# Optimization experiments

Measured on AMD Instinct MI355X. Metric: run time of the kernel, lower is better.

Reference implementation:

```python
import jax, jax.numpy as jnp
import numpy as np

HIDDEN = 2048
NUM_HEADS = 32
HEAD_DIM = 64
NUM_KV = 8
GROUP = NUM_HEADS // NUM_KV
SCALE = HEAD_DIM ** -0.5
ROPE_BASE = 10000.0


def apply_rope(t):
    # t: [B, H, S, D]; standard half-split rotary embedding
    S, D = t.shape[-2], t.shape[-1]
    inv_freq = 1.0 / (ROPE_BASE ** (jnp.arange(0, D, 2, dtype=jnp.float32) / D))  # [D/2]
    ang = jnp.arange(S, dtype=jnp.float32)[:, None] * inv_freq[None, :]           # [S, D/2]
    cos, sin = jnp.cos(ang), jnp.sin(ang)
    x1, x2 = t[..., : D // 2], t[..., D // 2 :]
    return jnp.concatenate([x1 * cos - x2 * sin, x2 * cos + x1 * sin], axis=-1)


def setup_inputs() -> dict:
    key = jax.random.key(0)
    ks = jax.random.split(key, 10)
    B, S = 2, 2048
    s_in = HIDDEN ** -0.5
    s_o = (NUM_HEADS * HEAD_DIM) ** -0.5
    return {
        "x": jax.random.normal(ks[0], (B, S, HIDDEN), jnp.float32),
        "Wq": jax.random.normal(ks[1], (NUM_HEADS * HEAD_DIM, HIDDEN), jnp.float32) * s_in,
        "bq": jnp.zeros((NUM_HEADS * HEAD_DIM,), jnp.float32),
        "Wk": jax.random.normal(ks[2], (NUM_KV * HEAD_DIM, HIDDEN), jnp.float32) * s_in,
        "bk": jnp.zeros((NUM_KV * HEAD_DIM,), jnp.float32),
        "Wv": jax.random.normal(ks[3], (NUM_KV * HEAD_DIM, HIDDEN), jnp.float32) * s_in,
        "bv": jnp.zeros((NUM_KV * HEAD_DIM,), jnp.float32),
        "Wo": jax.random.normal(ks[4], (HIDDEN, NUM_HEADS * HEAD_DIM), jnp.float32) * s_o,
        "bo": jnp.zeros((HIDDEN,), jnp.float32),
        "key_weights": jax.random.normal(ks[5], (NUM_HEADS,), jnp.float32),
    }


def reference(x, Wq, bq, Wk, bk, Wv, bv, Wo, bo, key_weights):
    B, S, _ = x.shape
    q = (x @ Wq.T + bq).reshape(B, S, NUM_HEADS, HEAD_DIM).transpose(0, 2, 1, 3)
    k = (x @ Wk.T + bk).reshape(B, S, NUM_KV, HEAD_DIM).transpose(0, 2, 1, 3)
    v = (x @ Wv.T + bv).reshape(B, S, NUM_KV, HEAD_DIM).transpose(0, 2, 1, 3)
    q = apply_rope(q)
    k = apply_rope(k)
    # group queries per KV head: [B, kv, g, S, D]
    qg = q.reshape(B, NUM_KV, GROUP, S, HEAD_DIM)
    scores = jnp.einsum("bkgsd,bktd->bkgst", qg, k) * SCALE
    scores = scores * key_weights.reshape(1, NUM_KV, GROUP, 1, 1)
    causal = jnp.tril(jnp.ones((S, S), bool))
    scores = jnp.where(causal, scores, -jnp.inf)
    a = jax.nn.softmax(scores, axis=-1)
    o = jnp.einsum("bkgst,bktd->bkgsd", a, v)  # [B, kv, g, S, D]
    o = o.reshape(B, NUM_HEADS, S, HEAD_DIM).transpose(0, 2, 1, 3).reshape(B, S, NUM_HEADS * HEAD_DIM)
    return o @ Wo.T + bo
```

## Files before the change

### kernel.cpp

```cpp
#include <hip/hip_runtime.h>
#include <stdint.h>

#define S_LEN 2048
#define HID   2048
#define NH    32
#define NKV   8
#define HD    64
#define BATCH 2
#define NROWS (BATCH * S_LEN)
#define QKVN  (NH*HD + 2*NKV*HD)

typedef unsigned short u16;
typedef __bf16 bf16_t;
typedef bf16_t bf16x8 __attribute__((ext_vector_type(8)));
typedef float  f32x4  __attribute__((ext_vector_type(4)));
typedef float  f32x16 __attribute__((ext_vector_type(16)));
typedef u16    u16x8  __attribute__((ext_vector_type(8)));

#define LOG2E 1.4426950408889634f

__device__ __forceinline__ u16 f2bf(float f) {
    union { float f; uint32_t u; } v; v.f = f;
    uint32_t u = v.u;
    return (u16)((u + 0x7fffu + ((u >> 16) & 1u)) >> 16);
}

__device__ __forceinline__ unsigned cvtpk(float a, float b) {
    unsigned r;
    asm("v_cvt_pk_bf16_f32 %0, %1, %2" : "=v"(r) : "v"(a), "v"(b));
    return r;
}

__device__ __forceinline__ void plswap(unsigned &a, unsigned &b) {
    asm volatile("v_permlane32_swap_b32 %0, %1" : "+v"(a), "+v"(b));
}

__device__ __forceinline__ void llds16(const void* g, void* l) {
    __builtin_amdgcn_global_load_lds(
        (const __attribute__((address_space(1))) void*)g,
        (__attribute__((address_space(3))) void*)l,
        16, 0, 0);
}

#define CBAR(N) do { \
    asm volatile("s_waitcnt vmcnt(" #N ")" ::: "memory"); \
    __builtin_amdgcn_s_barrier(); \
    __builtin_amdgcn_sched_barrier(0); \
} while (0)

#define CVT_GROUPS 2359296
__global__ void prep_all(const float* __restrict__ x, const float* __restrict__ wq,
                         const float* __restrict__ wk, const float* __restrict__ wv,
                         const float* __restrict__ wo,
                         const float* __restrict__ bq, const float* __restrict__ bk,
                         const float* __restrict__ bv,
                         u16* __restrict__ xb, u16* __restrict__ wqkvb, u16* __restrict__ wob,
                         float* __restrict__ rtab, float* __restrict__ bqkv) {
    int e = blockIdx.x * 256 + threadIdx.x;
    if (e < CVT_GROUPS) {
        const float* s; u16* d; int o;
        if (e < 1048576)      { s = x;  d = xb;                 o = e; }
        else if (e < 1572864) { s = wq; d = wqkvb;              o = e - 1048576; }
        else if (e < 1703936) { s = wk; d = wqkvb + 2048*2048;  o = e - 1572864; }
        else if (e < 1835008) { s = wv; d = wqkvb + 2560*2048;  o = e - 1703936; }
        else                  { s = wo; d = wob;                o = e - 1835008; }
        const float4* sp = (const float4*)s;
        float4 a = sp[2*(size_t)o], b = sp[2*(size_t)o + 1];
        u16x8 r;
        r[0]=f2bf(a.x); r[1]=f2bf(a.y); r[2]=f2bf(a.z); r[3]=f2bf(a.w);
        r[4]=f2bf(b.x); r[5]=f2bf(b.y); r[6]=f2bf(b.z); r[7]=f2bf(b.w);
        *(u16x8*)(d + 8*(size_t)o) = r;
    } else if (e < CVT_GROUPS + 65536) {
        int idx = e - CVT_GROUPS;
        int i = idx & 31, s = idx >> 5;
        float invf = exp2f(-(float)i * (13.287712379549449f / 32.0f));
        float ang = (float)s * invf;
        float sn, cs;
        sincosf(ang, &sn, &cs);
        rtab[idx] = cs;
        rtab[S_LEN*32 + idx] = sn;
    } else if (e < CVT_GROUPS + 65536 + QKVN) {
        int i = e - CVT_GROUPS - 65536;
        bqkv[i] = (i < 2048) ? bq[i] : (i < 2560 ? bk[i - 2048] : bv[i - 2560]);
    }
}


__global__ __launch_bounds__(256, 2) void gemm_qkv(
    const u16* __restrict__ A, const u16* __restrict__ Bw,
    const float* __restrict__ bias, const float* __restrict__ rtab,
    const float* __restrict__ kw,
    u16* __restrict__ qpk, u16* __restrict__ kpk, u16* __restrict__ vlin)
{
    const int M = NROWS, N = QKVN, K = HID;
    const int nbm = M >> 7, nbn = N >> 8;
    const int nwg = nbm * nbn;
    int wg = blockIdx.x;
    wg = (wg & 7) * (nwg >> 3) + (wg >> 3);
    const int bm = wg % nbm, bn = wg / nbm;
    const int brow = bm << 7, bcol = bn << 8;

    __shared__ u16 sbuf[3][12288];

    const int t = threadIdx.x;
    const int lane = t & 63, wid = t >> 6;
    const int wr = wid >> 1, wn = wid & 1;
    const int lr = lane & 15, lhi = lane >> 4;

    auto stage = [&](int kt, int bi) {
        const int k0 = kt << 5;
        #pragma unroll
        for (int i = 0; i < 2; ++i) {
            const unsigned off = ((unsigned)t << 4) + ((unsigned)i << 12);
            const unsigned row = off >> 6;
            const unsigned scb = (off & 63) ^ ((row & 3) << 4);
            llds16(A + (size_t)(brow + row) * K + (k0 + (scb >> 1)), &sbuf[bi][0] + (off >> 1));
        }
        #pragma unroll
        for (int i = 0; i < 4; ++i) {
            const unsigned off = ((unsigned)t << 4) + ((unsigned)i << 12);
            const unsigned row = off >> 6;
            const unsigned scb = (off & 63) ^ ((row & 3) << 4);
            llds16(Bw + (size_t)(bcol + row) * K + (k0 + (scb >> 1)), &sbuf[bi][4096] + (off >> 1));
        }
    };

    f32x4 acc[4][8] = {};
    const int nk = K >> 5;

    stage(0, 0);
    stage(1, 1);
    int cur = 0, st2 = 2;
    for (int kt = 0; kt < nk; ++kt) {
        if (kt < nk - 1) CBAR(6); else CBAR(0);
        if (kt + 2 < nk) stage(kt + 2, st2);
        const char* sA = (const char*)&sbuf[cur][0];
        const char* sB = (const char*)&sbuf[cur][4096];
        bf16x8 af[4], bfv[8];
        #pragma unroll
        for (int m = 0; m < 4; ++m) {
            const int row = wr*64 + m*16 + lr;
            af[m] = *(const bf16x8*)(sA + row*64 + ((lhi*16) ^ ((row & 3) << 4)));
        }
        #pragma unroll
        for (int n = 0; n < 8; ++n) {
            const int row = wn*128 + n*16 + lr;
            bfv[n] = *(const bf16x8*)(sB + row*64 + ((lhi*16) ^ ((row & 3) << 4)));
        }
        #pragma unroll
        for (int m = 0; m < 4; ++m)
            #pragma unroll
            for (int n = 0; n < 8; ++n)
                acc[m][n] = __builtin_amdgcn_mfma_f32_16x16x32_bf16(af[m], bfv[n], acc[m][n], 0, 0, 0);
        cur = (cur == 2) ? 0 : cur + 1;
        st2 = (st2 == 2) ? 0 : st2 + 1;
    }

    const int rowb = brow + wr*64;
    #pragma unroll
    for (int hg = 0; hg < 2; ++hg) {
        const int c64 = bcol + wn*128 + hg*64;
        const int hb  = c64 >> 6;
        if (hb < 40) {
            const bool isQ = hb < 32;
            const float sc = isQ ? (0.125f * LOG2E * kw[hb]) : 1.0f;
            u16* dst = isQ ? qpk : kpk;
            const int nheads = isQ ? 32 : 8;
            const int hloc = isQ ? hb : (hb - 32);
            #pragma unroll
            for (int m = 0; m < 4; ++m) {
                #pragma unroll
                for (int nn = 0; nn < 2; ++nn) {
                    const int n = 4*hg + nn;
                    const int i = nn*16 + lr;
                    const float b1 = bias[c64 + i];
                    const float b2 = bias[c64 + i + 32];
                    #pragma unroll
                    for (int j = 0; j < 4; ++j) {
                        const int row = rowb + m*16 + lhi*4 + j;
                        const int s = row & (S_LEN - 1);
                        const int bb = row >> 11;
                        const float x1 = acc[m][n][j] + b1;
                        const float x2 = acc[m][n+2][j] + b2;
                        const float cs = rtab[s*32 + i];
                        const float sn = rtab[S_LEN*32 + s*32 + i];
                        const size_t base = ((size_t)(bb*nheads + hloc)) * (S_LEN*64) + (size_t)s*64;
                        dst[base + i]      = f2bf((x1*cs - x2*sn) * sc);
                        dst[base + i + 32] = f2bf((x2*cs + x1*sn) * sc);
                    }
                }
            }
        } else {
            #pragma unroll
            for (int m = 0; m < 4; ++m) {
                #pragma unroll
                for (int nn = 0; nn < 4; ++nn) {
                    const int col = c64 + nn*16 + lr;
                    const float bv = bias[col];
                    #pragma unroll
                    for (int j = 0; j < 4; ++j) {
                        const int row = rowb + m*16 + lhi*4 + j;
                        vlin[(size_t)row * 512 + (col - 2560)] = f2bf(acc[m][nn + 4*hg][j] + bv);
                    }
                }
            }
        }
    }
}

__global__ __launch_bounds__(256, 2) void gemm_bt(
    const u16* __restrict__ A, const u16* __restrict__ Bw,
    const float* __restrict__ bias, float* __restrict__ C,
    int M, int N, int K)
{
    const int nbm = M >> 7, nbn = N >> 8;
    const int nwg = nbm * nbn;
    int wg = blockIdx.x;
    wg = (wg & 7) * (nwg >> 3) + (wg >> 3);
    const int bm = wg % nbm, bn = wg / nbm;
    const int brow = bm << 7, bcol = bn << 8;

    __shared__ u16 sbuf[3][12288];

    const int t = threadIdx.x;
    const int lane = t & 63, wid = t >> 6;
    const int wr = wid >> 1, wn = wid & 1;
    const int lr = lane & 15, lhi = lane >> 4;

    auto stage = [&](int kt, int bi) {
        const int k0 = kt << 5;
        #pragma unroll
        for (int i = 0; i < 2; ++i) {
            const unsigned off = ((unsigned)t << 4) + ((unsigned)i << 12);
            const unsigned row = off >> 6;
            const unsigned scb = (off & 63) ^ ((row & 3) << 4);
            llds16(A + (size_t)(brow + row) * K + (k0 + (scb >> 1)), &sbuf[bi][0] + (off >> 1));
        }
        #pragma unroll
        for (int i = 0; i < 4; ++i) {
            const unsigned off = ((unsigned)t << 4) + ((unsigned)i << 12);
            const unsigned row = off >> 6;
            const unsigned scb = (off & 63) ^ ((row & 3) << 4);
            llds16(Bw + (size_t)(bcol + row) * K + (k0 + (scb >> 1)), &sbuf[bi][4096] + (off >> 1));
        }
    };

    f32x4 acc[4][8] = {};
    const int nk = K >> 5;

    stage(0, 0);
    stage(1, 1);
    int cur = 0, st2 = 2;
    for (int kt = 0; kt < nk; ++kt) {
        if (kt < nk - 1) CBAR(6); else CBAR(0);
        if (kt + 2 < nk) stage(kt + 2, st2);
        const char* sA = (const char*)&sbuf[cur][0];
        const char* sB = (const char*)&sbuf[cur][4096];
        bf16x8 af[4], bfv[8];
        #pragma unroll
        for (int m = 0; m < 4; ++m) {
            const int row = wr*64 + m*16 + lr;
            af[m] = *(const bf16x8*)(sA + row*64 + ((lhi*16) ^ ((row & 3) << 4)));
        }
        #pragma unroll
        for (int n = 0; n < 8; ++n) {
            const int row = wn*128 + n*16 + lr;
            bfv[n] = *(const bf16x8*)(sB + row*64 + ((lhi*16) ^ ((row & 3) << 4)));
        }
        #pragma unroll
        for (int m = 0; m < 4; ++m)
            #pragma unroll
            for (int n = 0; n < 8; ++n)
                acc[m][n] = __builtin_amdgcn_mfma_f32_16x16x32_bf16(af[m], bfv[n], acc[m][n], 0, 0, 0);
        cur = (cur == 2) ? 0 : cur + 1;
        st2 = (st2 == 2) ? 0 : st2 + 1;
    }

    #pragma unroll
    for (int m = 0; m < 4; ++m) {
        #pragma unroll
        for (int n = 0; n < 8; ++n) {
            const int col = bcol + wn*128 + n*16 + lr;
            const float bv = bias[col];
            #pragma unroll
            for (int j = 0; j < 4; ++j) {
                const int row = brow + wr*64 + m*16 + lhi*4 + j;
                C[(size_t)row * N + col] = acc[m][n][j] + bv;
            }
        }
    }
}

__global__ void pack_vt(const u16* __restrict__ vlin, u16* __restrict__ vtb) {
    __shared__ u16 tile[64][67];
    const int st = blockIdx.x;
    const int bk = blockIdx.y;
    const int t = threadIdx.x;
    const int b = bk >> 3, kvh = bk & 7;
    const int r = t >> 2, cg = (t & 3) << 4;
    const u16* src = vlin + ((size_t)(b*S_LEN + st*64 + r)) * 512 + kvh*64 + cg;
    #pragma unroll
    for (int j = 0; j < 16; ++j) tile[r][cg + j] = src[j];
    __syncthreads();
    const int d = t >> 2, sg = (t & 3) << 4;
    u16* dst = vtb + ((size_t)(bk*64 + d)) * S_LEN + st*64 + sg;
    #pragma unroll
    for (int j = 0; j < 16; ++j) dst[j] = tile[sg + j][d];
}

__global__ __launch_bounds__(512, 4) void attn_fwd(
    const u16* __restrict__ Q,
    const u16* __restrict__ Kk,
    const u16* __restrict__ Vt,
    u16* __restrict__ O)
{
    __shared__ u16 sK[3][64 * 64];
    __shared__ u16 sV[3][64 * 64];

    const int t = threadIdx.x;
    const int lane = t & 63, wid = t >> 6;
    const int hi = lane >> 5, lq = lane & 31;
    const int bid = blockIdx.x;
    const int qb = (bid < 256) ? (7 - (bid >> 6)) : ((bid >> 6) - 4);
    const int bh = bid & 63;
    const int b = bh >> 5, h = bh & 31;
    const int kvh = h >> 2;

    const u16* Kp = Kk + ((size_t)(b*NKV + kvh)) * (S_LEN * 64);
    const u16* Vp = Vt + ((size_t)(b*NKV + kvh)) * (64 * S_LEN);

    const int q0w = qb*256 + wid*32;
    const int qg  = q0w + lq;

    const u16* Qrow = Q + (((size_t)bh) * S_LEN + qg) * 64 + 8*hi;
    bf16x8 qf[4];
    #pragma unroll
    for (int kd = 0; kd < 4; ++kd)
        qf[kd] = *(const bf16x8*)(Qrow + 16*kd);

    f32x16 accO0 = {}, accO1 = {};
    float m_run = 0.f, l_run = 0.f;

    const int ntB = 4*qb + 4;
    const int tmax_w = (q0w + 31) >> 6;

    auto stageKV = [&](int kt, int bi) {
        const int kv = kt << 6;
        const unsigned row = t >> 3, cb = (t & 7) << 4;
        const unsigned scb = cb ^ ((row & 7) << 4);
        llds16(Kp + (size_t)(kv + row) * 64 + (scb >> 1), &sK[bi][0] + t*8);
        llds16(Vp + (size_t)row * S_LEN + kv + (scb >> 1), &sV[bi][0] + t*8);
    };

    stageKV(0, 0);
    stageKV(1, 1);
    int cur = 0, st2 = 2;

    for (int tt = 0; tt < ntB; ++tt) {
        if (tt < ntB - 1) CBAR(2); else CBAR(0);
        if (tt + 2 < ntB) stageKV(tt + 2, st2);
        if (tt <= tmax_w) {
            const int kv0 = tt * 64;
            const float nm = -m_run;
            f32x16 s0, s1;
            #pragma unroll
            for (int r = 0; r < 16; ++r) { s0[r] = nm; s1[r] = nm; }
            #pragma unroll
            for (int kd = 0; kd < 4; ++kd) {
                const unsigned bc = ((unsigned)(32*kd + 16*hi)) ^ ((lq & 7) << 4);
                bf16x8 k0 = *(const bf16x8*)((const char*)&sK[cur][0] + lq*128 + bc);
                bf16x8 k1 = *(const bf16x8*)((const char*)&sK[cur][0] + (32 + lq)*128 + bc);
                s0 = __builtin_amdgcn_mfma_f32_32x32x16_bf16(k0, qf[kd], s0, 0, 0, 0);
                s1 = __builtin_amdgcn_mfma_f32_32x32x16_bf16(k1, qf[kd], s1, 0, 0, 0);
            }
            if (kv0 + 63 > q0w) {
                #pragma unroll
                for (int r = 0; r < 16; ++r) {
                    const int kvg = kv0 + (r & 3) + 8*(r >> 2) + 4*hi;
                    if (kvg > qg)      s0[r] = -INFINITY;
                    if (kvg + 32 > qg) s1[r] = -INFINITY;
                }
            }
            float mx[8];
            #pragma unroll
            for (int r = 0; r < 8; ++r)
                mx[r] = fmaxf(fmaxf(s0[r], s0[r+8]), fmaxf(s1[r], s1[r+8]));
            float tm = fmaxf(fmaxf(fmaxf(mx[0], mx[1]), fmaxf(mx[2], mx[3])),
                             fmaxf(fmaxf(mx[4], mx[5]), fmaxf(mx[6], mx[7])));
            tm = fmaxf(tm, __shfl_xor(tm, 32));
            if (!__all(tm <= 8.0f)) {
                const float dd = fmaxf(tm, 0.f);
                const float al = __builtin_amdgcn_exp2f(-dd);
                m_run += dd;
                l_run *= al;
                #pragma unroll
                for (int r = 0; r < 16; ++r) { accO0[r] *= al; accO1[r] *= al; }
                #pragma unroll
                for (int r = 0; r < 16; ++r) { s0[r] -= dd; s1[r] -= dd; }
            }
            #pragma unroll
            for (int r = 0; r < 16; ++r) {
                s0[r] = __builtin_amdgcn_exp2f(s0[r]);
                s1[r] = __builtin_amdgcn_exp2f(s1[r]);
            }
            float sm[8];
            #pragma unroll
            for (int r = 0; r < 8; ++r)
                sm[r] = (s0[r] + s0[r+8]) + (s1[r] + s1[r+8]);
            float rs = ((sm[0]+sm[1]) + (sm[2]+sm[3])) + ((sm[4]+sm[5]) + (sm[6]+sm[7]));
            rs += __shfl_xor(rs, 32);
            l_run += rs;

            #pragma unroll
            for (int ks = 0; ks < 4; ++ks) {
                const f32x16& e = (ks & 2) ? s1 : s0;
                const int rb = (ks & 1) * 8;
                unsigned x0 = cvtpk(e[rb + 0], e[rb + 1]);
                unsigned x1 = cvtpk(e[rb + 2], e[rb + 3]);
                unsigned y0 = cvtpk(e[rb + 4], e[rb + 5]);
                unsigned y1 = cvtpk(e[rb + 6], e[rb + 7]);
                plswap(x0, y0);
                plswap(x1, y1);
                union { unsigned u[4]; bf16x8 v; } pb;
                pb.u[0] = x0; pb.u[1] = x1; pb.u[2] = y0; pb.u[3] = y1;
                const unsigned bc = ((unsigned)(32*ks + 16*hi)) ^ ((lq & 7) << 4);
                bf16x8 v0 = *(const bf16x8*)((const char*)&sV[cur][0] + lq*128 + bc);
                bf16x8 v1 = *(const bf16x8*)((const char*)&sV[cur][0] + (32 + lq)*128 + bc);
                accO0 = __builtin_amdgcn_mfma_f32_32x32x16_bf16(v0, pb.v, accO0, 0, 0, 0);
                accO1 = __builtin_amdgcn_mfma_f32_32x32x16_bf16(v1, pb.v, accO1, 0, 0, 0);
            }
        }
        cur = (cur == 2) ? 0 : cur + 1;
        st2 = (st2 == 2) ? 0 : st2 + 1;
    }

    const float inv = 1.0f / l_run;
    u16* orow = O + (((size_t)(b * S_LEN) + q0w + lq)) * (NH*HD) + h*64;
    #pragma unroll
    for (int g = 0; g < 4; ++g) {
        uint2 w0, w1;
        w0.x = cvtpk(accO0[4*g + 0] * inv, accO0[4*g + 1] * inv);
        w0.y = cvtpk(accO0[4*g + 2] * inv, accO0[4*g + 3] * inv);
        *(uint2*)(orow + 8*g + 4*hi) = w0;
        w1.x = cvtpk(accO1[4*g + 0] * inv, accO1[4*g + 1] * inv);
        w1.y = cvtpk(accO1[4*g + 2] * inv, accO1[4*g + 3] * inv);
        *(uint2*)(orow + 32 + 8*g + 4*hi) = w1;
    }
}

extern "C" void kernel_launch(void* const* d_in, const int* in_sizes, int n_in,
                              void* d_out, int out_size, void* d_ws, size_t ws_size,
                              hipStream_t stream) {
    const float* x  = (const float*)d_in[0];
    const float* Wq = (const float*)d_in[1];
    const float* bq = (const float*)d_in[2];
    const float* Wk = (const float*)d_in[3];
    const float* bk = (const float*)d_in[4];
    const float* Wv = (const float*)d_in[5];
    const float* bv = (const float*)d_in[6];
    const float* Wo = (const float*)d_in[7];
    const float* bo = (const float*)d_in[8];
    const float* kw = (const float*)d_in[9];

    uint8_t* ws = (uint8_t*)d_ws;
    u16*   xb    = (u16*)(ws);
    u16*   wqkvb = (u16*)(ws + 16777216);
    u16*   wob   = (u16*)(ws + 29360128);
    u16*   qpk   = (u16*)(ws + 37748736);
    u16*   kpk   = (u16*)(ws + 54525952);
    u16*   vlin  = (u16*)(ws + 58720256);
    u16*   vtb   = (u16*)(ws + 62914560);
    u16*   ob    = (u16*)(ws + 67108864);
    float* bqkv  = (float*)(ws + 83886080);
    float* rtab  = (float*)(ws + 83898368);

    prep_all<<<9484, 256, 0, stream>>>(x, Wq, Wk, Wv, Wo, bq, bk, bv,
                                       xb, wqkvb, wob, rtab, bqkv);

    gemm_qkv<<<384, 256, 0, stream>>>(xb, wqkvb, bqkv, rtab, kw, qpk, kpk, vlin);

    pack_vt<<<dim3(32, 16), 256, 0, stream>>>(vlin, vtb);

    attn_fwd<<<dim3(512), dim3(512), 0, stream>>>(qpk, kpk, vtb, ob);

    gemm_bt<<<256, 256, 0, stream>>>(ob, wob, bo, (float*)d_out, NROWS, HID, HID);

    (void)in_sizes; (void)n_in; (void)out_size; (void)ws_size;
}
```

Before: 191.5 us.

## Split GEMM k-step into two phases interleaving global-to-LDS staging with MFMA

Both bf16 GEMM kernels now split each k-iteration into two halves. LDS fragment reads, the async global-to-LDS prefetch of the next-next tile (A plus one B chunk, then the remaining B chunks) and the MFMA blocks are interleaved, with barriers and lgkmcnt waits between them, and s_setprio raises wave priority around the MFMA bursts. The workgroup-to-tile mapping also changes from M-major to N-major. The attention kernel gets setprio around its MFMA loops. The goal is to hide load issue latency behind matrix math, at the cost of more barriers per iteration, which could add stalls.

New measurement: 185.0 us. 3.4% less time.

```diff
diff --git a/kernel.cpp b/kernel.cpp
--- a/kernel.cpp
+++ b/kernel.cpp
@@ -41,6 +41,10 @@
         (__attribute__((address_space(3))) void*)l,
         16, 0, 0);
 }
+
+#define LGKM0() do { asm volatile("s_waitcnt lgkmcnt(0)" ::: "memory"); \
+                     __builtin_amdgcn_sched_barrier(0); } while (0)
+#define BAR()   __builtin_amdgcn_s_barrier()
 
 #define CBAR(N) do { \
     asm volatile("s_waitcnt vmcnt(" #N ")" ::: "memory"); \
@@ -93,11 +97,11 @@
     u16* __restrict__ qpk, u16* __restrict__ kpk, u16* __restrict__ vlin)
 {
     const int M = NROWS, N = QKVN, K = HID;
-    const int nbm = M >> 7, nbn = N >> 8;
-    const int nwg = nbm * nbn;
+    const int nbn = N >> 8;
+    const int nwg = (M >> 7) * nbn;
     int wg = blockIdx.x;
     wg = (wg & 7) * (nwg >> 3) + (wg >> 3);
-    const int bm = wg % nbm, bn = wg / nbm;
+    const int bm = wg / nbn, bn = wg % nbn;
     const int brow = bm << 7, bcol = bn << 8;
 
     __shared__ u16 sbuf[3][12288];
@@ -107,7 +111,7 @@
     const int wr = wid >> 1, wn = wid & 1;
     const int lr = lane & 15, lhi = lane >> 4;
 
-    auto stage = [&](int kt, int bi) {
+    auto stageA = [&](int kt, int bi) {
         const int k0 = kt << 5;
         #pragma unroll
         for (int i = 0; i < 2; ++i) {
@@ -116,8 +120,17 @@
             const unsigned scb = (off & 63) ^ ((row & 3) << 4);
             llds16(A + (size_t)(brow + row) * K + (k0 + (scb >> 1)), &sbuf[bi][0] + (off >> 1));
         }
-        #pragma unroll
-        for (int i = 0; i < 4; ++i) {
+        {
+            const unsigned off = ((unsigned)t << 4);
+            const unsigned row = off >> 6;
+            const unsigned scb = (off & 63) ^ ((row & 3) << 4);
+            llds16(Bw + (size_t)(bcol + row) * K + (k0 + (scb >> 1)), &sbuf[bi][4096] + (off >> 1));
+        }
+    };
+    auto stageB = [&](int kt, int bi) {
+        const int k0 = kt << 5;
+        #pragma unroll
+        for (int i = 1; i < 4; ++i) {
             const unsigned off = ((unsigned)t << 4) + ((unsigned)i << 12);
             const unsigned row = off >> 6;
             const unsigned scb = (off & 63) ^ ((row & 3) << 4);
@@ -128,12 +141,13 @@
     f32x4 acc[4][8] = {};
     const int nk = K >> 5;
 
-    stage(0, 0);
-    stage(1, 1);
+    stageA(0, 0); stageB(0, 0);
+    stageA(1, 1); stageB(1, 1);
+    asm volatile("s_waitcnt vmcnt(6)" ::: "memory");
+    BAR();
+
     int cur = 0, st2 = 2;
     for (int kt = 0; kt < nk; ++kt) {
-        if (kt < nk - 1) CBAR(6); else CBAR(0);
-        if (kt + 2 < nk) stage(kt + 2, st2);
         const char* sA = (const char*)&sbuf[cur][0];
         const char* sB = (const char*)&sbuf[cur][4096];
         bf16x8 af[4], bfv[8];
@@ -143,15 +157,43 @@
             af[m] = *(const bf16x8*)(sA + row*64 + ((lhi*16) ^ ((row & 3) << 4)));
         }
         #pragma unroll
-        for (int n = 0; n < 8; ++n) {
+        for (int n = 0; n < 4; ++n) {
             const int row = wn*128 + n*16 + lr;
             bfv[n] = *(const bf16x8*)(sB + row*64 + ((lhi*16) ^ ((row & 3) << 4)));
         }
+        if (kt + 2 < nk) stageA(kt + 2, st2);
+        BAR();
+        LGKM0();
+        __builtin_amdgcn_s_setprio(1);
         #pragma unroll
         for (int m = 0; m < 4; ++m)
             #pragma unroll
-            for (int n = 0; n < 8; ++n)
+            for (int n = 0; n < 4; ++n)
                 acc[m][n] = __builtin_amdgcn_mfma_f32_16x16x32_bf16(af[m], bfv[n], acc[m][n], 0, 0, 0);
+        __builtin_amdgcn_s_setprio(0);
+        BAR();
+        #pragma unroll
+        for (int n = 4; n < 8; ++n) {
+            const int row = wn*128 + n*16 + lr;
+            bfv[n] = *(const bf16x8*)(sB + row*64 + ((lhi*16) ^ ((row & 3) << 4)));
+        }
+        if (kt + 2 < nk) stageB(kt + 2, st2);
+        BAR();
+        LGKM0();
+        __builtin_amdgcn_s_setprio(1);
+        #pragma unroll
+        for (int m = 0; m < 4; ++m)
+            #pragma unroll
+            for (int n = 4; n < 8; ++n)
+                acc[m][n] = __builtin_amdgcn_mfma_f32_16x16x32_bf16(af[m], bfv[n], acc[m][n], 0, 0, 0);
+        __builtin_amdgcn_s_setprio(0);
+        if (kt + 2 < nk) {
+            asm volatile("s_waitcnt vmcnt(6)" ::: "memory");
+            BAR();
+        } else if (kt + 1 < nk) {
+            asm volatile("s_waitcnt vmcnt(0)" ::: "memory");
+            BAR();
+        }
         cur = (cur == 2) ? 0 : cur + 1;
         st2 = (st2 == 2) ? 0 : st2 + 1;
     }
@@ -213,11 +255,11 @@
     const float* __restrict__ bias, float* __restrict__ C,
     int M, int N, int K)
 {
-    const int nbm = M >> 7, nbn = N >> 8;
-    const int nwg = nbm * nbn;
+    const int nbn = N >> 8;
+    const int nwg = (M >> 7) * nbn;
     int wg = blockIdx.x;
     wg = (wg & 7) * (nwg >> 3) + (wg >> 3);
-    const int bm = wg % nbm, bn = wg / nbm;
+    const int bm = wg / nbn, bn = wg % nbn;
     const int brow = bm << 7, bcol = bn << 8;
 
     __shared__ u16 sbuf[3][12288];
@@ -227,7 +269,7 @@
     const int wr = wid >> 1, wn = wid & 1;
     const int lr = lane & 15, lhi = lane >> 4;
 
-    auto stage = [&](int kt, int bi) {
+    auto stageA = [&](int kt, int bi) {
         const int k0 = kt << 5;
         #pragma unroll
         for (int i = 0; i < 2; ++i) {
@@ -236,8 +278,17 @@
             const unsigned scb = (off & 63) ^ ((row & 3) << 4);
             llds16(A + (size_t)(brow + row) * K + (k0 + (scb >> 1)), &sbuf[bi][0] + (off >> 1));
         }
-        #pragma unroll
-        for (int i = 0; i < 4; ++i) {
+        {
+            const unsigned off = ((unsigned)t << 4);
+            const unsigned row = off >> 6;
+            const unsigned scb = (off & 63) ^ ((row & 3) << 4);
+            llds16(Bw + (size_t)(bcol + row) * K + (k0 + (scb >> 1)), &sbuf[bi][4096] + (off >> 1));
+        }
+    };
+    auto stageB = [&](int kt, int bi) {
+        const int k0 = kt << 5;
+        #pragma unroll
+        for (int i = 1; i < 4; ++i) {
             const unsigned off = ((unsigned)t << 4) + ((unsigned)i << 12);
             const unsigned row = off >> 6;
             const unsigned scb = (off & 63) ^ ((row & 3) << 4);
@@ -248,12 +299,13 @@
     f32x4 acc[4][8] = {};
     const int nk = K >> 5;
 
-    stage(0, 0);
-    stage(1, 1);
+    stageA(0, 0); stageB(0, 0);
+    stageA(1, 1); stageB(1, 1);
+    asm volatile("s_waitcnt vmcnt(6)" ::: "memory");
+    BAR();
+
     int cur = 0, st2 = 2;
     for (int kt = 0; kt < nk; ++kt) {
-        if (kt < nk - 1) CBAR(6); else CBAR(0);
-        if (kt + 2 < nk) stage(kt + 2, st2);
         const char* sA = (const char*)&sbuf[cur][0];
         const char* sB = (const char*)&sbuf[cur][4096];
         bf16x8 af[4], bfv[8];
@@ -263,15 +315,43 @@
             af[m] = *(const bf16x8*)(sA + row*64 + ((lhi*16) ^ ((row & 3) << 4)));
         }
         #pragma unroll
-        for (int n = 0; n < 8; ++n) {
+        for (int n = 0; n < 4; ++n) {
             const int row = wn*128 + n*16 + lr;
             bfv[n] = *(const bf16x8*)(sB + row*64 + ((lhi*16) ^ ((row & 3) << 4)));
         }
+        if (kt + 2 < nk) stageA(kt + 2, st2);
+        BAR();
+        LGKM0();
+        __builtin_amdgcn_s_setprio(1);
         #pragma unroll
         for (int m = 0; m < 4; ++m)
             #pragma unroll
-            for (int n = 0; n < 8; ++n)
+            for (int n = 0; n < 4; ++n)
                 acc[m][n] = __builtin_amdgcn_mfma_f32_16x16x32_bf16(af[m], bfv[n], acc[m][n], 0, 0, 0);
+        __builtin_amdgcn_s_setprio(0);
+        BAR();
+        #pragma unroll
+        for (int n = 4; n < 8; ++n) {
+            const int row = wn*128 + n*16 + lr;
+            bfv[n] = *(const bf16x8*)(sB + row*64 + ((lhi*16) ^ ((row & 3) << 4)));
+        }
+        if (kt + 2 < nk) stageB(kt + 2, st2);
+        BAR();
+        LGKM0();
+        __builtin_amdgcn_s_setprio(1);
+        #pragma unroll
+        for (int m = 0; m < 4; ++m)
+            #pragma unroll
+            for (int n = 4; n < 8; ++n)
+                acc[m][n] = __builtin_amdgcn_mfma_f32_16x16x32_bf16(af[m], bfv[n], acc[m][n], 0, 0, 0);
+        __builtin_amdgcn_s_setprio(0);
+        if (kt + 2 < nk) {
+            asm volatile("s_waitcnt vmcnt(6)" ::: "memory");
+            BAR();
+        } else if (kt + 1 < nk) {
+            asm volatile("s_waitcnt vmcnt(0)" ::: "memory");
+            BAR();
+        }
         cur = (cur == 2) ? 0 : cur + 1;
         st2 = (st2 == 2) ? 0 : st2 + 1;
     }
@@ -365,6 +445,7 @@
             f32x16 s0, s1;
             #pragma unroll
             for (int r = 0; r < 16; ++r) { s0[r] = nm; s1[r] = nm; }
+            __builtin_amdgcn_s_setprio(1);
             #pragma unroll
             for (int kd = 0; kd < 4; ++kd) {
                 const unsigned bc = ((unsigned)(32*kd + 16*hi)) ^ ((lq & 7) << 4);
@@ -373,6 +454,7 @@
                 s0 = __builtin_amdgcn_mfma_f32_32x32x16_bf16(k0, qf[kd], s0, 0, 0, 0);
                 s1 = __builtin_amdgcn_mfma_f32_32x32x16_bf16(k1, qf[kd], s1, 0, 0, 0);
             }
+            __builtin_amdgcn_s_setprio(0);
             if (kv0 + 63 > q0w) {
                 #pragma unroll
                 for (int r = 0; r < 16; ++r) {
@@ -426,8 +508,10 @@
                 const unsigned bc = ((unsigned)(32*ks + 16*hi)) ^ ((lq & 7) << 4);
                 bf16x8 v0 = *(const bf16x8*)((const char*)&sV[cur][0] + lq*128 + bc);
                 bf16x8 v1 = *(const bf16x8*)((const char*)&sV[cur][0] + (32 + lq)*128 + bc);
+                __builtin_amdgcn_s_setprio(1);
                 accO0 = __builtin_amdgcn_mfma_f32_32x32x16_bf16(v0, pb.v, accO0, 0, 0, 0);
                 accO1 = __builtin_amdgcn_mfma_f32_32x32x16_bf16(v1, pb.v, accO1, 0, 0, 0);
+                __builtin_amdgcn_s_setprio(0);
             }
         }
         cur = (cur == 2) ? 0 : cur + 1;
```
